# Optimization experiments

Measured on AMD Instinct MI355X. Metric: run time of the kernel, lower is better.

Reference implementation:

```python
import jax, jax.numpy as jnp
import numpy as np

# db4 decomposition low-pass filter (pywt convention, 8 taps)
DEC_LO = np.array([-0.010597401784997278, 0.032883011666982945, 0.030841381835986965,
                   -0.18703481171888114, -0.02798376941698385, 0.6308807679295904,
                   0.7148465705525415, 0.23037781330885523], dtype=np.float32)
L = DEC_LO.shape[0]  # 8
REC_LO = DEC_LO[::-1].copy()
DEC_HI = (REC_LO * ((-1.0) ** (np.arange(L) + 1))).astype(np.float32)
REC_HI = DEC_HI[::-1].copy()
LEVEL = 7

# lax.conv does correlation; flip filters to get true convolution (pywt semantics)
K_DEC = jnp.asarray(np.stack([DEC_LO[::-1], DEC_HI[::-1]])[:, None, :])  # [2,1,L] out-ch: (lo, hi)
K_REC = jnp.asarray(np.stack([REC_LO[::-1], REC_HI[::-1]])[None, :, :])  # [1,2,L] in-ch: (ca, cd)


def dwt(x):
    # x: [B, N]. pywt zero-mode dwt == full conv then take odd indices;
    # fused here as stride-2 conv with asymmetric padding (L-2, L-1).
    y = jax.lax.conv_general_dilated(x[:, None, :], K_DEC, (2,), [(L - 2, L - 1)])
    return y[:, 0], y[:, 1]  # each [B, floor((N+L-1)/2)]


def idwt(ca, cd):
    # upsample-by-2 (lhs_dilation, length 2n-1), full conv, trim L-2 each side -> pad (1,1)
    y = jax.lax.conv_general_dilated(jnp.stack([ca, cd], axis=1), K_REC, (1,),
                                     [(1, 1)], lhs_dilation=(2,))
    return y[:, 0]  # [B, 2n - L + 2]


def soft(c, t):
    # pywt.threshold(mode='soft')
    return jnp.sign(c) * jnp.maximum(jnp.abs(c) - t, 0.0)


def setup_inputs() -> dict:
    key = jax.random.key(0)
    k1, k2 = jax.random.split(key)
    x = jax.random.normal(k1, (32768, 1116), dtype=jnp.float32)
    # learned scalar parameter, initialized like nn.Parameter(torch.tensor(0.02))
    raw_threshold = jnp.asarray(0.02, dtype=jnp.float32)
    return {"x": x, "raw_threshold": raw_threshold}


def reference(x, raw_threshold):
    thr = jnp.maximum(raw_threshold, 0.01)  # torch.clamp(min=0.01)
    # wavedec: 7-level analysis
    a = x
    details = []
    for _ in range(LEVEL):
        a, d = dwt(a)
        details.append(d)
    # soft-threshold every coefficient band (including approximation)
    a = soft(a, thr)
    details = [soft(d, thr) for d in details]
    # waverec: synthesis, truncating cA when one sample longer than cD (pywt rule)
    for d in reversed(details):
        if a.shape[-1] > d.shape[-1]:
            a = a[:, : d.shape[-1]]
        a = idwt(a, d)
    return a  # [B, 1116]
```

## Files before the change

kernel.cpp:

```cpp
#include <hip/hip_runtime.h>

#define NCOL 1116
#define NLEV 7
#define NT 256

static __device__ __forceinline__ float softf(float c, float t) {
    float m = fabsf(c) - t;
    return m > 0.0f ? copysignf(m, c) : 0.0f;
}

__global__ __launch_bounds__(NT)
void wavelet_kernel(const float* __restrict__ x,
                    const float* __restrict__ thr_ptr,
                    float* __restrict__ out) {
    constexpr float DEC_LO[8] = {-0.010597401784997278f,  0.032883011666982945f,
                                  0.030841381835986965f, -0.18703481171888114f,
                                 -0.02798376941698385f,   0.6308807679295904f,
                                  0.7148465705525415f,    0.23037781330885523f};
    constexpr float DEC_HI[8] = {-0.23037781330885523f,   0.7148465705525415f,
                                 -0.6308807679295904f,   -0.02798376941698385f,
                                  0.18703481171888114f,   0.030841381835986965f,
                                 -0.032883011666982945f, -0.010597401784997278f};
    constexpr float REC_LO[8] = { 0.23037781330885523f,   0.7148465705525415f,
                                  0.6308807679295904f,   -0.02798376941698385f,
                                 -0.18703481171888114f,   0.030841381835986965f,
                                  0.032883011666982945f, -0.010597401784997278f};
    constexpr float REC_HI[8] = {-0.010597401784997278f, -0.032883011666982945f,
                                  0.030841381835986965f,  0.18703481171888114f,
                                 -0.02798376941698385f,  -0.6308807679295904f,
                                  0.7148465705525415f,   -0.23037781330885523f};

    constexpr int alen[8] = {1116, 561, 284, 145, 76, 41, 24, 15};
    constexpr int doff[7] = {0, 561, 845, 990, 1066, 1107, 1131};

    __shared__ float A[1132];
    __shared__ float B[578];
    __shared__ float D[1146];

    const int tid = threadIdx.x;
    const int row = blockIdx.x;
    const float thr = fmaxf(thr_ptr[0], 0.01f);

    float* a0 = A + 8;
    float* b0 = B + 8;

    {
        const float4* xr = (const float4*)(x + (size_t)row * NCOL);
        float4* dst = (float4*)a0;
        for (int i = tid; i < NCOL / 4; i += NT) dst[i] = xr[i];
        if (tid < 8) { A[tid] = 0.0f; a0[NCOL + tid] = 0.0f; }
    }
    __syncthreads();

    float* cur = a0;
    float* nxt = b0;
    #pragma unroll
    for (int l = 0; l < NLEV; ++l) {
        const int nout = alen[l + 1];
        float* dp = D + doff[l];
        for (int o = tid; o < nout; o += NT) {
            const float* src = cur + 2 * o + 1;
            float lo = 0.0f, hi = 0.0f;
            #pragma unroll
            for (int s = 0; s < 8; ++s) {
                float v = src[-s];
                lo = fmaf(DEC_LO[s], v, lo);
                hi = fmaf(DEC_HI[s], v, hi);
            }
            nxt[o] = lo;
            dp[o] = softf(hi, thr);
        }
        if (tid < 8) { nxt[-8 + tid] = 0.0f; nxt[nout + tid] = 0.0f; }
        float* t = cur; cur = nxt; nxt = t;
        __syncthreads();
    }

    if (tid < 15) cur[tid] = softf(cur[tid], thr);
    __syncthreads();

    #pragma unroll
    for (int l = NLEV - 1; l >= 0; --l) {
        const int M = alen[l + 1];
        const float* dp = D + doff[l];
        const int npair = M - 3;
        if (l > 0) {
            for (int m = tid; m < npair; m += NT) {
                float ca0 = cur[m], ca1 = cur[m + 1], ca2 = cur[m + 2], ca3 = cur[m + 3];
                float cd0 = dp[m],  cd1 = dp[m + 1],  cd2 = dp[m + 2],  cd3 = dp[m + 3];
                float y0 = fmaf(REC_LO[0], ca3, fmaf(REC_LO[2], ca2, fmaf(REC_LO[4], ca1, REC_LO[6] * ca0)));
                y0 = fmaf(REC_HI[0], cd3, fmaf(REC_HI[2], cd2, fmaf(REC_HI[4], cd1, fmaf(REC_HI[6], cd0, y0))));
                float y1 = fmaf(REC_LO[1], ca3, fmaf(REC_LO[3], ca2, fmaf(REC_LO[5], ca1, REC_LO[7] * ca0)));
                y1 = fmaf(REC_HI[1], cd3, fmaf(REC_HI[3], cd2, fmaf(REC_HI[5], cd1, fmaf(REC_HI[7], cd0, y1))));
                nxt[2 * m] = y0;
                nxt[2 * m + 1] = y1;
            }
            float* t = cur; cur = nxt; nxt = t;
            __syncthreads();
        } else {
            float2* orow = (float2*)(out + (size_t)row * NCOL);
            for (int m = tid; m < npair; m += NT) {
                float ca0 = cur[m], ca1 = cur[m + 1], ca2 = cur[m + 2], ca3 = cur[m + 3];
                float cd0 = dp[m],  cd1 = dp[m + 1],  cd2 = dp[m + 2],  cd3 = dp[m + 3];
                float y0 = fmaf(REC_LO[0], ca3, fmaf(REC_LO[2], ca2, fmaf(REC_LO[4], ca1, REC_LO[6] * ca0)));
                y0 = fmaf(REC_HI[0], cd3, fmaf(REC_HI[2], cd2, fmaf(REC_HI[4], cd1, fmaf(REC_HI[6], cd0, y0))));
                float y1 = fmaf(REC_LO[1], ca3, fmaf(REC_LO[3], ca2, fmaf(REC_LO[5], ca1, REC_LO[7] * ca0)));
                y1 = fmaf(REC_HI[1], cd3, fmaf(REC_HI[3], cd2, fmaf(REC_HI[5], cd1, fmaf(REC_HI[7], cd0, y1))));
                orow[m] = make_float2(y0, y1);
            }
        }
    }
}

extern "C" void kernel_launch(void* const* d_in, const int* in_sizes, int n_in,
                              void* d_out, int out_size, void* d_ws, size_t ws_size,
                              hipStream_t stream) {
    const float* x = (const float*)d_in[0];
    const float* thr = (const float*)d_in[1];
    float* out = (float*)d_out;
    const int nrow = in_sizes[0] / NCOL;
    hipLaunchKernelGGL(wavelet_kernel, dim3(nrow), dim3(NT), 0, stream, x, thr, out);
}
```

Baseline: 266.5 us.

## Compute two outputs per thread with vectorized LDS loads and packed FMA

Each thread in both the forward and inverse wavelet levels now produces two adjacent outputs, loading a 12-float window with float4 LDS reads and accumulating with 2-wide vector FMAs that can map to packed FP32 instructions. Shared buffers are realigned (pad of 6, even detail offsets) so the vector loads and stores are aligned. The approximation threshold is folded into the last forward level, which removes one barrier. The aim is fewer LDS transactions and instructions per output, at the cost of more complex indexing and odd-length edge handling.

```diff
diff --git a/kernel.cpp b/kernel.cpp
--- a/kernel.cpp
+++ b/kernel.cpp
@@ -1,114 +1,157 @@
 #include <hip/hip_runtime.h>
 
+#define NT 256
 #define NCOL 1116
 #define NLEV 7
-#define NT 256
+
+typedef float v2f __attribute__((ext_vector_type(2)));
+
+static constexpr float DEC_LO[8] = {-0.010597401784997278f,  0.032883011666982945f,
+                                     0.030841381835986965f, -0.18703481171888114f,
+                                    -0.02798376941698385f,   0.6308807679295904f,
+                                     0.7148465705525415f,    0.23037781330885523f};
+static constexpr float DEC_HI[8] = {-0.23037781330885523f,   0.7148465705525415f,
+                                    -0.6308807679295904f,   -0.02798376941698385f,
+                                     0.18703481171888114f,   0.030841381835986965f,
+                                    -0.032883011666982945f, -0.010597401784997278f};
+static constexpr float REC_LO[8] = { 0.23037781330885523f,   0.7148465705525415f,
+                                     0.6308807679295904f,   -0.02798376941698385f,
+                                    -0.18703481171888114f,   0.030841381835986965f,
+                                     0.032883011666982945f, -0.010597401784997278f};
+static constexpr float REC_HI[8] = {-0.010597401784997278f, -0.032883011666982945f,
+                                     0.030841381835986965f,  0.18703481171888114f,
+                                    -0.02798376941698385f,  -0.6308807679295904f,
+                                     0.7148465705525415f,   -0.23037781330885523f};
+
+static constexpr int ALEN[8] = {1116, 561, 284, 145, 76, 41, 24, 15};
+static constexpr int DOFF[7] = {0, 562, 846, 992, 1068, 1110, 1136};
 
 static __device__ __forceinline__ float softf(float c, float t) {
     float m = fabsf(c) - t;
     return m > 0.0f ? copysignf(m, c) : 0.0f;
 }
 
+static __device__ __forceinline__ v2f vfma(float c, v2f v, v2f a) {
+#if __has_builtin(__builtin_elementwise_fma)
+    return __builtin_elementwise_fma((v2f){c, c}, v, a);
+#else
+    v2f r; r.x = fmaf(c, v.x, a.x); r.y = fmaf(c, v.y, a.y); return r;
+#endif
+}
+
+template <int L, bool LAST>
+static __device__ __forceinline__ void fwd_level(const float* cur, float* nxt, float* dp,
+                                                 float thr, int tid) {
+    constexpr int nout = ALEN[L + 1];
+    constexpr int ntask = (nout + 1) / 2;
+    for (int t = tid; t < ntask; t += NT) {
+        const float* src = cur + 4 * t - 6;
+        float4 w0 = *(const float4*)src;
+        float4 w1 = *(const float4*)(src + 4);
+        float4 w2 = *(const float4*)(src + 8);
+        float w[12] = {w0.x, w0.y, w0.z, w0.w, w1.x, w1.y, w1.z, w1.w,
+                       w2.x, w2.y, w2.z, w2.w};
+        v2f lo = {0.f, 0.f}, hi = {0.f, 0.f};
+#pragma unroll
+        for (int s = 0; s < 8; ++s) {
+            v2f v = {w[7 - s], w[9 - s]};
+            lo = vfma(DEC_LO[s], v, lo);
+            hi = vfma(DEC_HI[s], v, hi);
+        }
+        if (LAST) { lo.x = softf(lo.x, thr); lo.y = softf(lo.y, thr); }
+        hi.x = softf(hi.x, thr);
+        hi.y = softf(hi.y, thr);
+        *(v2f*)(dp + 2 * t) = hi;
+        if (!(nout & 1) || (2 * t + 1 < nout)) {
+            *(v2f*)(nxt + 2 * t) = lo;
+        } else {
+            nxt[2 * t] = lo.x;
+        }
+    }
+    if (!LAST) {
+        if (tid < 6) nxt[-6 + tid] = 0.0f;
+        if (tid < 10) nxt[nout + tid] = 0.0f;
+    }
+}
+
+template <int L, bool FINAL>
+static __device__ __forceinline__ void inv_level(const float* ca, const float* dp,
+                                                 float* y, int tid) {
+    constexpr int M = ALEN[L + 1];
+    constexpr int npair = M - 3;
+    constexpr int ntask = (npair + 1) / 2;
+    for (int t = tid; t < ntask; t += NT) {
+        const float* cap = ca + 2 * t;
+        const float* ddp = dp + 2 * t;
+        float2 a01 = *(const float2*)cap;
+        float2 a23 = *(const float2*)(cap + 2);
+        float  a4  = cap[4];
+        float2 d01 = *(const float2*)ddp;
+        float2 d23 = *(const float2*)(ddp + 2);
+        float  d4  = ddp[4];
+        float aw[5] = {a01.x, a01.y, a23.x, a23.y, a4};
+        float dw[5] = {d01.x, d01.y, d23.x, d23.y, d4};
+        v2f ye = {0.f, 0.f}, yo = {0.f, 0.f};
+#pragma unroll
+        for (int k = 0; k < 4; ++k) {
+            v2f va = {aw[3 - k], aw[4 - k]};
+            v2f vd = {dw[3 - k], dw[4 - k]};
+            ye = vfma(REC_LO[2 * k],     va, ye);
+            yo = vfma(REC_LO[2 * k + 1], va, yo);
+            ye = vfma(REC_HI[2 * k],     vd, ye);
+            yo = vfma(REC_HI[2 * k + 1], vd, yo);
+        }
+        if (FINAL) {
+            *(float4*)(y + 4 * t) = make_float4(ye.x, yo.x, ye.y, yo.y);
+        } else {
+            *(v2f*)(y + 4 * t)     = (v2f){ye.x, yo.x};
+            *(v2f*)(y + 4 * t + 2) = (v2f){ye.y, yo.y};
+        }
+    }
+}
+
 __global__ __launch_bounds__(NT)
 void wavelet_kernel(const float* __restrict__ x,
                     const float* __restrict__ thr_ptr,
                     float* __restrict__ out) {
-    constexpr float DEC_LO[8] = {-0.010597401784997278f,  0.032883011666982945f,
-                                  0.030841381835986965f, -0.18703481171888114f,
-                                 -0.02798376941698385f,   0.6308807679295904f,
-                                  0.7148465705525415f,    0.23037781330885523f};
-    constexpr float DEC_HI[8] = {-0.23037781330885523f,   0.7148465705525415f,
-                                 -0.6308807679295904f,   -0.02798376941698385f,
-                                  0.18703481171888114f,   0.030841381835986965f,
-                                 -0.032883011666982945f, -0.010597401784997278f};
-    constexpr float REC_LO[8] = { 0.23037781330885523f,   0.7148465705525415f,
-                                  0.6308807679295904f,   -0.02798376941698385f,
-                                 -0.18703481171888114f,   0.030841381835986965f,
-                                  0.032883011666982945f, -0.010597401784997278f};
-    constexpr float REC_HI[8] = {-0.010597401784997278f, -0.032883011666982945f,
-                                  0.030841381835986965f,  0.18703481171888114f,
-                                 -0.02798376941698385f,  -0.6308807679295904f,
-                                  0.7148465705525415f,   -0.23037781330885523f};
-
-    constexpr int alen[8] = {1116, 561, 284, 145, 76, 41, 24, 15};
-    constexpr int doff[7] = {0, 561, 845, 990, 1066, 1107, 1131};
-
-    __shared__ float A[1132];
-    __shared__ float B[578];
-    __shared__ float D[1146];
+    __shared__ __align__(16) float A[1136];
+    __shared__ __align__(16) float B[580];
+    __shared__ __align__(16) float D[1154];
 
     const int tid = threadIdx.x;
-    const int row = blockIdx.x;
     const float thr = fmaxf(thr_ptr[0], 0.01f);
-
-    float* a0 = A + 8;
-    float* b0 = B + 8;
+    float* a0 = A + 6;
+    float* b0 = B + 6;
 
     {
-        const float4* xr = (const float4*)(x + (size_t)row * NCOL);
-        float4* dst = (float4*)a0;
-        for (int i = tid; i < NCOL / 4; i += NT) dst[i] = xr[i];
-        if (tid < 8) { A[tid] = 0.0f; a0[NCOL + tid] = 0.0f; }
+        const float4* xr = (const float4*)(x + (size_t)blockIdx.x * NCOL);
+        for (int i = tid; i < NCOL / 4; i += NT) {
+            float4 v = xr[i];
+            *(v2f*)(a0 + 4 * i)     = (v2f){v.x, v.y};
+            *(v2f*)(a0 + 4 * i + 2) = (v2f){v.z, v.w};
+        }
+        if (tid < 6)  A[tid] = 0.0f;
+        if (tid < 10) a0[NCOL + tid] = 0.0f;
     }
     __syncthreads();
 
-    float* cur = a0;
-    float* nxt = b0;
-    #pragma unroll
-    for (int l = 0; l < NLEV; ++l) {
-        const int nout = alen[l + 1];
-        float* dp = D + doff[l];
-        for (int o = tid; o < nout; o += NT) {
-            const float* src = cur + 2 * o + 1;
-            float lo = 0.0f, hi = 0.0f;
-            #pragma unroll
-            for (int s = 0; s < 8; ++s) {
-                float v = src[-s];
-                lo = fmaf(DEC_LO[s], v, lo);
-                hi = fmaf(DEC_HI[s], v, hi);
-            }
-            nxt[o] = lo;
-            dp[o] = softf(hi, thr);
-        }
-        if (tid < 8) { nxt[-8 + tid] = 0.0f; nxt[nout + tid] = 0.0f; }
-        float* t = cur; cur = nxt; nxt = t;
-        __syncthreads();
-    }
+    fwd_level<0, false>(a0, b0, D + DOFF[0], thr, tid); __syncthreads();
+    fwd_level<1, false>(b0, a0, D + DOFF[1], thr, tid); __syncthreads();
+    fwd_level<2, false>(a0, b0, D + DOFF[2], thr, tid); __syncthreads();
+    fwd_level<3, false>(b0, a0, D + DOFF[3], thr, tid); __syncthreads();
+    fwd_level<4, false>(a0, b0, D + DOFF[4], thr, tid); __syncthreads();
+    fwd_level<5, false>(b0, a0, D + DOFF[5], thr, tid); __syncthreads();
+    fwd_level<6, true >(a0, b0, D + DOFF[6], thr, tid); __syncthreads();
 
-    if (tid < 15) cur[tid] = softf(cur[tid], thr);
-    __syncthreads();
+    inv_level<6, false>(b0, D + DOFF[6], a0, tid); __syncthreads();
+    inv_level<5, false>(a0, D + DOFF[5], b0, tid); __syncthreads();
+    inv_level<4, false>(b0, D + DOFF[4], a0, tid); __syncthreads();
+    inv_level<3, false>(a0, D + DOFF[3], b0, tid); __syncthreads();
+    inv_level<2, false>(b0, D + DOFF[2], a0, tid); __syncthreads();
+    inv_level<1, false>(a0, D + DOFF[1], b0, tid); __syncthreads();
 
-    #pragma unroll
-    for (int l = NLEV - 1; l >= 0; --l) {
-        const int M = alen[l + 1];
-        const float* dp = D + doff[l];
-        const int npair = M - 3;
-        if (l > 0) {
-            for (int m = tid; m < npair; m += NT) {
-                float ca0 = cur[m], ca1 = cur[m + 1], ca2 = cur[m + 2], ca3 = cur[m + 3];
-                float cd0 = dp[m],  cd1 = dp[m + 1],  cd2 = dp[m + 2],  cd3 = dp[m + 3];
-                float y0 = fmaf(REC_LO[0], ca3, fmaf(REC_LO[2], ca2, fmaf(REC_LO[4], ca1, REC_LO[6] * ca0)));
-                y0 = fmaf(REC_HI[0], cd3, fmaf(REC_HI[2], cd2, fmaf(REC_HI[4], cd1, fmaf(REC_HI[6], cd0, y0))));
-                float y1 = fmaf(REC_LO[1], ca3, fmaf(REC_LO[3], ca2, fmaf(REC_LO[5], ca1, REC_LO[7] * ca0)));
-                y1 = fmaf(REC_HI[1], cd3, fmaf(REC_HI[3], cd2, fmaf(REC_HI[5], cd1, fmaf(REC_HI[7], cd0, y1))));
-                nxt[2 * m] = y0;
-                nxt[2 * m + 1] = y1;
-            }
-            float* t = cur; cur = nxt; nxt = t;
-            __syncthreads();
-        } else {
-            float2* orow = (float2*)(out + (size_t)row * NCOL);
-            for (int m = tid; m < npair; m += NT) {
-                float ca0 = cur[m], ca1 = cur[m + 1], ca2 = cur[m + 2], ca3 = cur[m + 3];
-                float cd0 = dp[m],  cd1 = dp[m + 1],  cd2 = dp[m + 2],  cd3 = dp[m + 3];
-                float y0 = fmaf(REC_LO[0], ca3, fmaf(REC_LO[2], ca2, fmaf(REC_LO[4], ca1, REC_LO[6] * ca0)));
-                y0 = fmaf(REC_HI[0], cd3, fmaf(REC_HI[2], cd2, fmaf(REC_HI[4], cd1, fmaf(REC_HI[6], cd0, y0))));
-                float y1 = fmaf(REC_LO[1], ca3, fmaf(REC_LO[3], ca2, fmaf(REC_LO[5], ca1, REC_LO[7] * ca0)));
-                y1 = fmaf(REC_HI[1], cd3, fmaf(REC_HI[3], cd2, fmaf(REC_HI[5], cd1, fmaf(REC_HI[7], cd0, y1))));
-                orow[m] = make_float2(y0, y1);
-            }
-        }
-    }
+    float* orow = out + (size_t)blockIdx.x * NCOL;
+    inv_level<0, true>(b0, D + DOFF[0], orow, tid);
 }
 
 extern "C" void kernel_launch(void* const* d_in, const int* in_sizes, int n_in,
```

Measured after the change: 277.6 us. 1.04x slower.
